# Performance work log

Measured on AMD Instinct MI355X. Metric: run time of the kernel, lower is better.

Reference implementation:

```python
import jax, jax.numpy as jnp
import numpy as np

N, N_SPINS, N_HIDDEN = 8192, 1024, 1024


def setup_inputs() -> dict:
    key = jax.random.key(0)
    ks = jax.random.split(key, 6)
    s_in = 1.0 / np.sqrt(N_SPINS)
    s_h = 1.0 / np.sqrt(N_HIDDEN)
    return {
        "x": jax.random.normal(ks[0], (N, N_SPINS), dtype=jnp.float32),
        "W_in": jax.random.normal(ks[1], (N_HIDDEN, N_SPINS), dtype=jnp.float32) * s_in,
        "b_in": jax.random.normal(ks[2], (N_HIDDEN,), dtype=jnp.float32) * s_in,
        "Wq": jax.random.normal(ks[3], (N_HIDDEN, N_HIDDEN), dtype=jnp.float32) * s_h,
        "Wk": jax.random.normal(ks[4], (N_HIDDEN, N_HIDDEN), dtype=jnp.float32) * s_h,
        "Wv": jax.random.normal(ks[5], (N_HIDDEN, N_HIDDEN), dtype=jnp.float32) * s_h,
    }


def reference(x, W_in, b_in, Wq, Wk, Wv):
    # embedding: Linear(n_spins, n_hidden)  -> h: [N, H]
    h = x @ W_in.T + b_in
    q = h @ Wq.T                      # [N, H]
    k = h @ Wk.T                      # [N, H]
    v = h @ Wv.T                      # [N, H]
    scores = (q @ k.T) * 0.25         # [N, N], scale 1/4 as in source
    attn = jax.nn.softmax(scores, axis=0)  # softmax over dim=0 (columns)
    out = attn @ v                    # [N, H]
    # log(cosh(z)) = |z| + log1p(exp(-2|z|)) - log(2), numerically stable
    a = jnp.abs(out)
    logcosh = a + jnp.log1p(jnp.exp(-2.0 * a)) - jnp.log(jnp.asarray(2.0, out.dtype))
    return jnp.sum(logcosh, axis=-1)  # [N]
```

## Files before the change

kernel.cpp:

```cpp
#include <hip/hip_runtime.h>
#include <hip/hip_bf16.h>
#include <cstdint>
#include <cstddef>

#define NTOK 8192
#define NHID 1024

typedef __attribute__((ext_vector_type(8))) __bf16 bf16x8;
typedef __attribute__((ext_vector_type(4))) float f32x4;

__device__ __forceinline__ unsigned short f2bf(float f) {
    union { float f; unsigned u; } v; v.f = f;
    unsigned r = v.u + 0x7FFF + ((v.u >> 16) & 1);
    return (unsigned short)(r >> 16);
}

__device__ __forceinline__ float bf2f(unsigned short u) {
    union { unsigned u; float f; } v; v.u = ((unsigned)u) << 16;
    return v.f;
}

__device__ __forceinline__ void async_copy16(const void* gsrc, void* ldsdst) {
    __builtin_amdgcn_global_load_lds(
        (const __attribute__((address_space(1))) unsigned int*)gsrc,
        (__attribute__((address_space(3))) unsigned int*)ldsdst,
        16, 0, 0);
}

template <int EPI, bool SWAP>
__global__ __launch_bounds__(256) void gemm_bt(
    const unsigned short* __restrict__ A,
    const unsigned short* __restrict__ B,
    void* __restrict__ C,
    const float* __restrict__ bias,
    float* __restrict__ zsum,
    float scale, int M, int N, int K, int lda, int ldb)
{
    __shared__ __attribute__((aligned(16))) unsigned short As[128 * 64];
    __shared__ __attribute__((aligned(16))) unsigned short Bs[128 * 64];

    const int tid  = threadIdx.x;
    const int wave = tid >> 6;
    const int lane = tid & 63;
    const int bm = (SWAP ? blockIdx.x : blockIdx.y) * 128;
    const int bn = (SWAP ? blockIdx.y : blockIdx.x) * 128;
    const size_t ldaz = (size_t)lda;
    const size_t ldbz = (size_t)ldb;

    const int srow = lane >> 3;
    const int scol = ((lane & 7) ^ srow) * 8;
    const unsigned short* Ag[4];
    const unsigned short* Bg[4];
    unsigned short* Al[4];
    unsigned short* Bl[4];
#pragma unroll
    for (int t = 0; t < 4; ++t) {
        int r = (wave * 4 + t) * 8 + srow;
        Ag[t] = A + (size_t)(bm + r) * ldaz + scol;
        Bg[t] = B + (size_t)(bn + r) * ldbz + scol;
        Al[t] = &As[(wave * 4 + t) * 512];
        Bl[t] = &Bs[(wave * 4 + t) * 512];
    }

    const int wm = (wave >> 1) * 64;
    const int wn = (wave & 1) * 64;
    const int fr = lane & 15;
    const int frl = fr & 7;
    const int q = lane >> 4;

    f32x4 acc[4][4] = {};

    for (int kt = 0; kt < K; kt += 64) {
#pragma unroll
        for (int t = 0; t < 4; ++t) {
            async_copy16(Ag[t], Al[t]);
            async_copy16(Bg[t], Bl[t]);
            Ag[t] += 64;
            Bg[t] += 64;
        }
        __syncthreads();
#pragma unroll
        for (int ks = 0; ks < 2; ++ks) {
            const int pc = ((ks * 4 + q) ^ frl) * 8;
            bf16x8 a[4], b[4];
#pragma unroll
            for (int i = 0; i < 4; ++i) {
                a[i] = *(const bf16x8*)&As[(wm + i * 16 + fr) * 64 + pc];
                b[i] = *(const bf16x8*)&Bs[(wn + i * 16 + fr) * 64 + pc];
            }
#pragma unroll
            for (int i = 0; i < 4; ++i)
#pragma unroll
                for (int j = 0; j < 4; ++j)
                    acc[i][j] = __builtin_amdgcn_mfma_f32_16x16x32_bf16(
                        a[i], b[j], acc[i][j], 0, 0, 0);
        }
        __syncthreads();
    }

    const int erow = q * 4;
#pragma unroll
    for (int j = 0; j < 4; ++j) {
        const int gcol = bn + wn + j * 16 + fr;
        const float bv = (EPI == 1 && bias) ? bias[gcol] : 0.0f;
        float colsum = 0.0f;
#pragma unroll
        for (int i = 0; i < 4; ++i) {
            const int grow0 = bm + wm + i * 16 + erow;
#pragma unroll
            for (int r = 0; r < 4; ++r) {
                float v;
                if (EPI == 2) {
                    v = __expf(fmaf(acc[i][j][r], scale, -64.0f));
                    colsum += v;
                } else {
                    v = acc[i][j][r] * scale + bv;
                }
                size_t idx = (size_t)(grow0 + r) * N + gcol;
                if (EPI == 0) ((float*)C)[idx] = v;
                else          ((unsigned short*)C)[idx] = f2bf(v);
            }
        }
        if (EPI == 2) {
            colsum += __shfl_xor(colsum, 16, 64);
            colsum += __shfl_xor(colsum, 32, 64);
            if (q == 0) atomicAdd(&zsum[gcol], colsum);
        }
    }
}

__global__ void cvt_all(const float4* __restrict__ x,
                        const float4* __restrict__ w0,
                        const float4* __restrict__ w1,
                        const float4* __restrict__ w2,
                        const float4* __restrict__ w3,
                        ushort4* __restrict__ xb,
                        ushort4* __restrict__ wdst,
                        float4* __restrict__ pz4,
                        int n4x, int n4w)
{
    int i = blockIdx.x * blockDim.x + threadIdx.x;
    int n4 = n4x + 4 * n4w;
    if (i >= n4) {
        int zi = i - n4;
        if (zi < 2048) pz4[zi] = make_float4(0.f, 0.f, 0.f, 0.f);
        return;
    }
    float4 f;
    ushort4* dst;
    if (i < n4x) {
        f = x[i]; dst = xb + i;
    } else {
        int r = i - n4x;
        int seg = r / n4w, off = r % n4w;
        const float4* src = (seg == 0) ? w0 : (seg == 1) ? w1 : (seg == 2) ? w2 : w3;
        f = src[off]; dst = wdst + r;
    }
    ushort4 o;
    o.x = f2bf(f.x); o.y = f2bf(f.y); o.z = f2bf(f.z); o.w = f2bf(f.w);
    *dst = o;
}

__global__ __launch_bounds__(256) void transpose_scale(
    const unsigned short* __restrict__ v,
    const float* __restrict__ z,
    unsigned short* __restrict__ vt)
{
    __shared__ float lds[64 * 65];
    const int tid = threadIdx.x;
    const int j0 = blockIdx.x * 64;
    const int h0 = blockIdx.y * 64;
    const int c = tid & 63;
    const int r0 = tid >> 6;
#pragma unroll
    for (int it = 0; it < 16; ++it) {
        int r = it * 4 + r0;
        lds[r * 65 + c] = bf2f(v[(size_t)(j0 + r) * 3072 + h0 + c]);
    }
    __syncthreads();
    const float rz = 1.0f / z[j0 + c];
#pragma unroll
    for (int it = 0; it < 16; ++it) {
        int r = it * 4 + r0;
        vt[(size_t)(h0 + r) * NTOK + j0 + c] = f2bf(lds[c * 65 + r] * rz);
    }
}

__global__ void logcosh_rowsum(const ushort4* __restrict__ O4,
                               float* __restrict__ out)
{
    const float LN2 = 0.69314718055994531f;
    int row = blockIdx.x;
    ushort4 u = O4[(size_t)row * 256 + threadIdx.x];
    float s = 0.0f, a;
    a = fabsf(bf2f(u.x)); s += a + log1pf(__expf(-2.0f * a));
    a = fabsf(bf2f(u.y)); s += a + log1pf(__expf(-2.0f * a));
    a = fabsf(bf2f(u.z)); s += a + log1pf(__expf(-2.0f * a));
    a = fabsf(bf2f(u.w)); s += a + log1pf(__expf(-2.0f * a));
    s -= 4.0f * LN2;
    for (int off = 32; off; off >>= 1) s += __shfl_down(s, off, 64);
    __shared__ float red[4];
    if ((threadIdx.x & 63) == 0) red[threadIdx.x >> 6] = s;
    __syncthreads();
    if (threadIdx.x == 0) out[row] = red[0] + red[1] + red[2] + red[3];
}

extern "C" void kernel_launch(void* const* d_in, const int* in_sizes, int n_in,
                              void* d_out, int out_size, void* d_ws, size_t ws_size,
                              hipStream_t stream)
{
    (void)in_sizes; (void)n_in; (void)out_size; (void)ws_size;

    const float* x    = (const float*)d_in[0];
    const float* W_in = (const float*)d_in[1];
    const float* b_in = (const float*)d_in[2];
    const float* Wq   = (const float*)d_in[3];
    const float* Wk   = (const float*)d_in[4];
    const float* Wv   = (const float*)d_in[5];
    float* out = (float*)d_out;

    char* w = (char*)d_ws;
    const size_t MiB = 1024 * 1024;
    unsigned short* Pb     = (unsigned short*)(w);
    unsigned short* qkv    = (unsigned short*)(w + 128 * MiB);
    unsigned short* xb     = (unsigned short*)(w + 128 * MiB);
    unsigned short* outb   = (unsigned short*)(w + 128 * MiB);
    unsigned short* hb     = (unsigned short*)(w + 176 * MiB);
    unsigned short* vtb    = (unsigned short*)(w + 176 * MiB);
    unsigned short* wib    = (unsigned short*)(w + 192 * MiB);
    unsigned short* wqkvb  = (unsigned short*)(w + 194 * MiB);
    float*          pz     = (float*)         (w + 200 * MiB);

    {
        int n4x = NTOK * NHID / 4;
        int n4w = NHID * NHID / 4;
        int n4  = n4x + 4 * n4w;
        cvt_all<<<n4 / 256 + 8, 256, 0, stream>>>(
            (const float4*)x, (const float4*)W_in, (const float4*)Wq,
            (const float4*)Wk, (const float4*)Wv,
            (ushort4*)xb, (ushort4*)wib, (float4*)pz, n4x, n4w);
    }

    dim3 gNH(NHID / 128, NTOK / 128);
    gemm_bt<1, false><<<gNH, 256, 0, stream>>>(
        xb, wib, hb, b_in, nullptr, 1.0f, NTOK, NHID, NHID, NHID, NHID);

    dim3 gQKV(3 * NHID / 128, NTOK / 128);
    gemm_bt<1, false><<<gQKV, 256, 0, stream>>>(
        hb, wqkvb, qkv, nullptr, nullptr, 1.0f, NTOK, 3 * NHID, NHID, NHID, NHID);

    dim3 gS(NTOK / 128, NTOK / 128);
    gemm_bt<2, false><<<gS, 256, 0, stream>>>(
        qkv, qkv + NHID, Pb, nullptr, pz, 0.25f, NTOK, NTOK, NHID,
        3 * NHID, 3 * NHID);

    dim3 gT(NTOK / 64, NHID / 64);
    transpose_scale<<<gT, 256, 0, stream>>>(qkv + 2 * NHID, pz, vtb);

    dim3 gO(NTOK / 128, NHID / 128);
    gemm_bt<1, true><<<gO, 256, 0, stream>>>(
        Pb, vtb, outb, nullptr, nullptr, 1.0f, NTOK, NHID, NTOK, NTOK, NTOK);

    logcosh_rowsum<<<NTOK, 256, 0, stream>>>((const ushort4*)outb, out);
}
```

Before: 533.9 us.

## Use 256x128 tiles with 512 threads and triple-buffered async LDS pipeline

The GEMM kernel moves from 128x128 tiles with 4 waves to 256x128 tiles with 8 waves, and loads K-slices into a three-stage LDS ring using async global-to-LDS copies with partial vmcnt waits. This lets loads for later stages overlap with MFMA work and replaces two barriers per iteration with one. MFMA sections run at raised wave priority through s_setprio. The trade-offs are 144KB of LDS per block, which limits occupancy, and half as many blocks for the smaller GEMMs.

```diff
diff --git a/kernel.cpp b/kernel.cpp
--- a/kernel.cpp
+++ b/kernel.cpp
@@ -28,7 +28,7 @@
 }
 
 template <int EPI, bool SWAP>
-__global__ __launch_bounds__(256) void gemm_bt(
+__global__ __launch_bounds__(512, 2) void gemm_bt2(
     const unsigned short* __restrict__ A,
     const unsigned short* __restrict__ B,
     void* __restrict__ C,
@@ -36,13 +36,12 @@
     float* __restrict__ zsum,
     float scale, int M, int N, int K, int lda, int ldb)
 {
-    __shared__ __attribute__((aligned(16))) unsigned short As[128 * 64];
-    __shared__ __attribute__((aligned(16))) unsigned short Bs[128 * 64];
+    __shared__ __attribute__((aligned(16))) unsigned short lds[3][24576];
 
     const int tid  = threadIdx.x;
     const int wave = tid >> 6;
     const int lane = tid & 63;
-    const int bm = (SWAP ? blockIdx.x : blockIdx.y) * 128;
+    const int bm = (SWAP ? blockIdx.x : blockIdx.y) * 256;
     const int bn = (SWAP ? blockIdx.y : blockIdx.x) * 128;
     const size_t ldaz = (size_t)lda;
     const size_t ldbz = (size_t)ldb;
@@ -50,16 +49,19 @@
     const int srow = lane >> 3;
     const int scol = ((lane & 7) ^ srow) * 8;
     const unsigned short* Ag[4];
-    const unsigned short* Bg[4];
-    unsigned short* Al[4];
-    unsigned short* Bl[4];
+    const unsigned short* Bg[2];
+    int Aoff[4], Boff[2];
 #pragma unroll
     for (int t = 0; t < 4; ++t) {
         int r = (wave * 4 + t) * 8 + srow;
         Ag[t] = A + (size_t)(bm + r) * ldaz + scol;
+        Aoff[t] = (wave * 4 + t) * 512;
+    }
+#pragma unroll
+    for (int t = 0; t < 2; ++t) {
+        int r = (wave * 2 + t) * 8 + srow;
         Bg[t] = B + (size_t)(bn + r) * ldbz + scol;
-        Al[t] = &As[(wave * 4 + t) * 512];
-        Bl[t] = &Bs[(wave * 4 + t) * 512];
+        Boff[t] = 16384 + (wave * 2 + t) * 512;
     }
 
     const int wm = (wave >> 1) * 64;
@@ -70,15 +72,30 @@
 
     f32x4 acc[4][4] = {};
 
-    for (int kt = 0; kt < K; kt += 64) {
-#pragma unroll
-        for (int t = 0; t < 4; ++t) {
-            async_copy16(Ag[t], Al[t]);
-            async_copy16(Bg[t], Bl[t]);
-            Ag[t] += 64;
-            Bg[t] += 64;
-        }
-        __syncthreads();
+    const int nt = K >> 6;
+
+    auto stage = [&](int s) {
+        unsigned short* base = &lds[s][0];
+#pragma unroll
+        for (int t = 0; t < 4; ++t) { async_copy16(Ag[t], base + Aoff[t]); Ag[t] += 64; }
+#pragma unroll
+        for (int t = 0; t < 2; ++t) { async_copy16(Bg[t], base + Boff[t]); Bg[t] += 64; }
+    };
+
+    stage(0);
+    stage(1);
+    asm volatile("s_waitcnt vmcnt(6)" ::: "memory");
+    __builtin_amdgcn_s_barrier();
+
+    int cb = 0;
+    int sb = 2;
+    for (int t = 0; t < nt; ++t) {
+        if (t + 2 < nt) {
+            stage(sb);
+            sb = (sb == 2) ? 0 : sb + 1;
+        }
+        const unsigned short* As = &lds[cb][0];
+        const unsigned short* Bs = &lds[cb][16384];
 #pragma unroll
         for (int ks = 0; ks < 2; ++ks) {
             const int pc = ((ks * 4 + q) ^ frl) * 8;
@@ -88,14 +105,21 @@
                 a[i] = *(const bf16x8*)&As[(wm + i * 16 + fr) * 64 + pc];
                 b[i] = *(const bf16x8*)&Bs[(wn + i * 16 + fr) * 64 + pc];
             }
+            __builtin_amdgcn_s_setprio(1);
 #pragma unroll
             for (int i = 0; i < 4; ++i)
 #pragma unroll
                 for (int j = 0; j < 4; ++j)
                     acc[i][j] = __builtin_amdgcn_mfma_f32_16x16x32_bf16(
                         a[i], b[j], acc[i][j], 0, 0, 0);
-        }
-        __syncthreads();
+            __builtin_amdgcn_s_setprio(0);
+        }
+        if (t < nt - 1) {
+            if (t < nt - 2) asm volatile("s_waitcnt vmcnt(6)" ::: "memory");
+            else            asm volatile("s_waitcnt vmcnt(0)" ::: "memory");
+            __builtin_amdgcn_s_barrier();
+            cb = (cb == 2) ? 0 : cb + 1;
+        }
     }
 
     const int erow = q * 4;
@@ -241,24 +265,24 @@
             (ushort4*)xb, (ushort4*)wib, (float4*)pz, n4x, n4w);
     }
 
-    dim3 gNH(NHID / 128, NTOK / 128);
-    gemm_bt<1, false><<<gNH, 256, 0, stream>>>(
+    dim3 gNH(NHID / 128, NTOK / 256);
+    gemm_bt2<1, false><<<gNH, 512, 0, stream>>>(
         xb, wib, hb, b_in, nullptr, 1.0f, NTOK, NHID, NHID, NHID, NHID);
 
-    dim3 gQKV(3 * NHID / 128, NTOK / 128);
-    gemm_bt<1, false><<<gQKV, 256, 0, stream>>>(
+    dim3 gQKV(3 * NHID / 128, NTOK / 256);
+    gemm_bt2<1, false><<<gQKV, 512, 0, stream>>>(
         hb, wqkvb, qkv, nullptr, nullptr, 1.0f, NTOK, 3 * NHID, NHID, NHID, NHID);
 
-    dim3 gS(NTOK / 128, NTOK / 128);
-    gemm_bt<2, false><<<gS, 256, 0, stream>>>(
+    dim3 gS(NTOK / 128, NTOK / 256);
+    gemm_bt2<2, false><<<gS, 512, 0, stream>>>(
         qkv, qkv + NHID, Pb, nullptr, pz, 0.25f, NTOK, NTOK, NHID,
         3 * NHID, 3 * NHID);
 
     dim3 gT(NTOK / 64, NHID / 64);
     transpose_scale<<<gT, 256, 0, stream>>>(qkv + 2 * NHID, pz, vtb);
 
-    dim3 gO(NTOK / 128, NHID / 128);
-    gemm_bt<1, true><<<gO, 256, 0, stream>>>(
+    dim3 gO(NTOK / 256, NHID / 128);
+    gemm_bt2<1, true><<<gO, 512, 0, stream>>>(
         Pb, vtb, outb, nullptr, nullptr, 1.0f, NTOK, NHID, NTOK, NTOK, NTOK);
 
     logcosh_rowsum<<<NTOK, 256, 0, stream>>>((const ushort4*)outb, out);
```

New measurement: 483.5 us. 9.5% less time.
